# Performance work log

Hardware: AMD Instinct MI355X
Metric: run time of the kernel (lower is better)

## Reference

```python
import jax, jax.numpy as jnp
import numpy as np

N, L, M, NNZ, P, G, H = 4096, 64, 256, 100000, 3, 1, 8
D = M // H  # head_dim = 32


def setup_inputs() -> dict:
    key = jax.random.key(0)
    ks = jax.random.split(key, 8)
    return {
        "sparse_values": jax.random.normal(ks[0], (NNZ, M), jnp.float32),
        "linear_index": jax.random.randint(ks[1], (N, L), 0, NNZ, jnp.int32),
        "is_specified": jax.random.randint(ks[2], (N, L), 0, 2, jnp.int32).astype(bool),
        "query": jax.random.normal(ks[3], (N, M), jnp.float32),
        "key_weight": jax.random.normal(ks[4], (M, M), jnp.float32) * 0.05,
        "value_weight": jax.random.normal(ks[5], (M, M), jnp.float32) * 0.05,
        "key_positions": jax.random.uniform(ks[6], (N, L, P), jnp.float32),
        "rope_freqs": jax.random.normal(ks[7], (P, G, H, D // 2), jnp.float32),
        "n_heads": H,
    }


def reference(sparse_values, linear_index, is_specified, query, key_weight,
              value_weight, key_positions, rope_freqs, n_heads):
    n, l = linear_index.shape
    m = query.shape[-1]
    h = n_heads
    d = m // h
    scale = 1.0 / np.sqrt(m)  # docstring: default scale_factor = 1/sqrt(M)

    # Gather each query's key subset; unspecified keys -> 0 (will be masked)
    safe_idx = jnp.where(is_specified, linear_index, 0)
    gathered = jnp.where(is_specified[..., None], sparse_values[safe_idx], 0.0)  # [N,L,M]

    # Key / value projections (nn.Linear convention: x @ W.T)
    k = (gathered @ key_weight.T).reshape(n, l, h, d)
    v = (gathered @ value_weight.T).reshape(n, l, h, d)

    # RoPE on keys: angles [N,L,H,D/2], summed over position dims P and freq groups G
    angles = jnp.einsum('nlp,pghd->nlhd', key_positions, rope_freqs)
    cos, sin = jnp.cos(angles), jnp.sin(angles)
    k_even, k_odd = k[..., 0::2], k[..., 1::2]
    k = jnp.stack([k_even * cos - k_odd * sin,
                   k_even * sin + k_odd * cos], axis=-1).reshape(n, l, h, d)

    # Per-query subset attention (query is pre-rotated per docstring)
    q = query.reshape(n, h, d)
    scores = jnp.einsum('nhd,nlhd->nhl', q, k) * scale
    scores = jnp.where(is_specified[:, None, :], scores, -jnp.inf)

    # Queries with all keys unspecified -> zero output (avoid NaN from all -inf)
    any_spec = is_specified.any(axis=-1)  # [N]
    attn = jax.nn.softmax(jnp.where(any_spec[:, None, None], scores, 0.0), axis=-1)
    out = jnp.einsum('nhl,nlhd->nhd', attn, v).reshape(n, m)
    out = jnp.where(any_spec[:, None], out, 0.0)
    return out, is_specified
```

## Files before the change

kernel.cpp:

```cpp
#include <hip/hip_runtime.h>
#include <math.h>

#define N_Q 4096
#define L_K 64
#define M_D 256

typedef float f32x16 __attribute__((ext_vector_type(16)));
typedef __bf16 b16x8 __attribute__((ext_vector_type(8)));
union F8 { uint4 u; unsigned short s[8]; b16x8 v; };

__device__ __forceinline__ unsigned short f2bf(float x) {
  unsigned u = __float_as_uint(x);
  return (unsigned short)((u + 0x7fffu + ((u >> 16) & 1u)) >> 16);
}

__global__ __launch_bounds__(256) void k_prep(const unsigned char* __restrict__ raw,
                                              float* __restrict__ out2,
                                              const float* __restrict__ wv,
                                              float* __restrict__ wvt,
                                              const float* __restrict__ wk,
                                              unsigned short* __restrict__ wkf,
                                              const int* __restrict__ lin,
                                              int* __restrict__ pcnt,
                                              int* __restrict__ plin,
                                              unsigned char* __restrict__ pl) {
  __shared__ int pll_s[256];
  __shared__ unsigned char pls_s[256];
  __shared__ int pc_s[4];
  const int tid = threadIdx.x, lane = tid & 63;
  pll_s[tid] = 0;
  pls_s[tid] = 0;
  int v = 0;
  for (int i = tid; i < 4096; i += 256)
    if (i & 3) v |= raw[i];
  int f = __syncthreads_or(v);
  const int gi = blockIdx.x * 256 + tid;
  bool b = f ? (raw[gi] != 0) : (((const int*)raw)[gi] != 0);
  out2[gi] = b ? 1.0f : 0.0f;
  int li = lin[gi];
  unsigned long long mask = __ballot(b);
  if (b) {
    int rank = __popcll(mask & ((1ull << lane) - 1));
    pll_s[(tid & 192) + rank] = li;
    pls_s[(tid & 192) + rank] = (unsigned char)lane;
  }
  if (lane == 0) pc_s[tid >> 6] = __popcll(mask);
  __syncthreads();
  plin[gi] = pll_s[tid];
  pl[gi] = pls_s[tid];
  if (tid < 4) pcnt[blockIdx.x * 4 + tid] = pc_s[tid];

  if (gi < 65536) {
    wvt[(gi & 255) * 256 + (gi >> 8)] = wv[gi];
    int oc = gi >> 8, k = gi & 255;
    int tt = oc >> 5, c32o = oc & 31;
    int ks = k >> 4, kg2 = (k >> 3) & 1, j = k & 7;
    wkf[(((tt * 16 + ks) << 6) + kg2 * 32 + c32o) * 8 + j] = f2bf(wk[gi]);
  }
}

#define SC_OFF  65536
#define AT_OFF  (SC_OFF + 4096)
#define LDS_SZ  (AT_OFF + 4096)

__global__ __launch_bounds__(512, 4) void k_fused2(
    const float* __restrict__ sv, const float* __restrict__ q,
    const unsigned short* __restrict__ wkf, const float* __restrict__ pos,
    const float* __restrict__ freqs, const int* __restrict__ pcnt,
    const int* __restrict__ plin, const unsigned char* __restrict__ pl,
    unsigned short* __restrict__ agg) {
  __shared__ __align__(16) char smem[LDS_SZ];
  float* sc_s   = (float*)(smem + SC_OFF);
  float* attn_s = (float*)(smem + AT_OFF);
  const int tid = threadIdx.x, lane = tid & 63, w = tid >> 6;
  const int c32 = lane & 31, kg = lane >> 5;
  const int rt = w >> 1, ch = w & 1;
  const int n0g = blockIdx.x * 2;
  const int cnt0 = pcnt[n0g], cnt1 = pcnt[n0g + 1];
  const int cpair = cnt0 + cnt1;

  if (cpair == 0) {
    #pragma unroll
    for (int i = tid; i < 1024; i += 512)
      *(ushort4*)(agg + (size_t)n0g * 2048 + i * 4) = ushort4{0, 0, 0, 0};
    return;
  }
  const int ct32 = (cpair + 31) & ~31;
  const int ntiles = ct32 >> 5;

  {
    const int r0 = tid >> 5, ii = tid & 31;
    #pragma unroll
    for (int pp = 0; pp < 8; ++pp) {
      const int rloc = pp * 16 + r0;
      if (rloc < ct32) {
        const int pe = (rloc < cpair) ? rloc : (cpair - 1);
        const int src = (pe < cnt0) ? plin[n0g * 64 + pe]
                                    : plin[(n0g + 1) * 64 + (pe - cnt0)];
        const float* rp = sv + (size_t)src * 256 + ii * 8;
        float4 f0 = *(const float4*)rp;
        float4 f1 = *(const float4*)(rp + 4);
        F8 pk;
        pk.s[0] = f2bf(f0.x); pk.s[1] = f2bf(f0.y); pk.s[2] = f2bf(f0.z); pk.s[3] = f2bf(f0.w);
        pk.s[4] = f2bf(f1.x); pk.s[5] = f2bf(f1.y); pk.s[6] = f2bf(f1.z); pk.s[7] = f2bf(f1.w);
        *(uint4*)(smem + rloc * 512 + ((ii ^ (rloc & 31)) << 4)) = pk.u;
      }
    }
  }
  __syncthreads();

  if (rt < ntiles) {
    f32x16 acc[4];
    #pragma unroll
    for (int t = 0; t < 4; ++t)
      #pragma unroll
      for (int r = 0; r < 16; ++r) acc[t][r] = 0.0f;

    const char* fbase = (const char*)wkf + ch * 65536 + lane * 16;
    F8 afc[4], afn[4];
    #pragma unroll
    for (int t = 0; t < 4; ++t) afc[t].u = *(const uint4*)(fbase + (t * 16) * 1024);

    #pragma unroll
    for (int ks = 0; ks < 16; ++ks) {
      if (ks < 15) {
        #pragma unroll
        for (int t = 0; t < 4; ++t)
          afn[t].u = *(const uint4*)(fbase + (t * 16 + ks + 1) * 1024);
      }
      F8 bf;
      bf.u = *(const uint4*)(smem + (rt * 32 + c32) * 512 + ((((ks << 1) + kg) ^ c32) << 4));
      #pragma unroll
      for (int t = 0; t < 4; ++t)
        acc[t] = __builtin_amdgcn_mfma_f32_32x32x16_bf16(afc[t].v, bf.v, acc[t], 0, 0, 0);
      #pragma unroll
      for (int t = 0; t < 4; ++t) afc[t] = afn[t];
    }

    const int p = rt * 32 + c32;
    const bool pv = p < cpair;
    const int pe = pv ? p : (cpair - 1);
    const int nl = (pe >= cnt0) ? 1 : 0;
    const int n_g = n0g + nl;
    const int l = pl[n_g * 64 + (pe - (nl ? cnt0 : 0))];
    const float* lp = pos + ((size_t)n_g * 64 + l) * 3;
    const float pp0 = lp[0], pp1 = lp[1], pp2 = lp[2];
    #pragma unroll
    for (int t = 0; t < 4; ++t) {
      const int h = ch * 4 + t;
      const float* qh = q + (size_t)n_g * 256 + h * 32;
      const float* F = freqs + h * 16;
      float s = 0.f;
      #pragma unroll
      for (int g = 0; g < 4; ++g) {
        #pragma unroll
        for (int pr = 0; pr < 2; ++pr) {
          const int d0 = g * 8 + kg * 4 + pr * 2;
          const int jj = d0 >> 1;
          const int r = g * 4 + pr * 2;
          float ke = acc[t][r], ko = acc[t][r + 1];
          float ang = pp0 * F[jj] + pp1 * F[128 + jj] + pp2 * F[256 + jj];
          float sn, cs;
          __sincosf(ang, &sn, &cs);
          float2 qq = *(const float2*)(qh + d0);
          s += ke * (cs * qq.x + sn * qq.y) + ko * (cs * qq.y - sn * qq.x);
        }
      }
      s += __shfl_xor(s, 32);
      if (kg == 0 && pv) sc_s[p * 8 + h] = s * 0.0625f;
    }
  }
  __syncthreads();

  #pragma unroll
  for (int uu = 0; uu < 2; ++uu) {
    const int unit = w * 2 + uu;
    const int nl = unit >> 3, h = unit & 7;
    const int start = nl ? cnt0 : 0;
    const int cn = nl ? cnt1 : cnt0;
    const bool vl = lane < cn;
    float v = vl ? sc_s[(start + lane) * 8 + h] : -__builtin_inff();
    float mx = v;
    #pragma unroll
    for (int o = 32; o; o >>= 1) mx = fmaxf(mx, __shfl_xor(mx, o));
    float e = vl ? __expf(v - mx) : 0.f;
    float sm = e;
    #pragma unroll
    for (int o = 32; o; o >>= 1) sm += __shfl_xor(sm, o);
    if (vl) attn_s[(start + lane) * 8 + h] = e / sm;
  }
  __syncthreads();

  const int m = tid & 255, hh = tid >> 8;
  const int start = hh ? cnt0 : 0;
  const int cn = hh ? cnt1 : cnt0;
  const int n_g = n0g + hh;
  float ga[8];
  #pragma unroll
  for (int h = 0; h < 8; ++h) ga[h] = 0.f;
  for (int p2 = 0; p2 < cn; ++p2) {
    const int prow = start + p2;
    unsigned short us = *(const unsigned short*)(smem + prow * 512 +
                        ((((m >> 3) ^ (prow & 31)) << 4) | ((m & 7) << 1)));
    float gv = __uint_as_float((unsigned)us << 16);
    const float4* ap = (const float4*)(attn_s + prow * 8);
    float4 aA = ap[0], aB = ap[1];
    ga[0] += aA.x * gv; ga[1] += aA.y * gv; ga[2] += aA.z * gv; ga[3] += aA.w * gv;
    ga[4] += aB.x * gv; ga[5] += aB.y * gv; ga[6] += aB.z * gv; ga[7] += aB.w * gv;
  }
  #pragma unroll
  for (int h = 0; h < 8; ++h)
    agg[(size_t)n_g * 2048 + h * 256 + m] = f2bf(ga[h]);
}

__global__ __launch_bounds__(256) void k_out(const unsigned short* __restrict__ agg,
                                             const float* __restrict__ wvt,
                                             float* __restrict__ out) {
  __shared__ float a_s[4][8][260];
  const int tid = threadIdx.x;
  const int n0 = blockIdx.x * 4;
  #pragma unroll
  for (int it = 0; it < 4; ++it) {
    uint4 v = *(const uint4*)(agg + (size_t)(n0 + it) * 2048 + tid * 8);
    const unsigned short* sp = (const unsigned short*)&v;
    const int hh = tid >> 5, m0 = (tid & 31) * 8;
    #pragma unroll
    for (int k2 = 0; k2 < 8; ++k2)
      a_s[it][hh][m0 + k2] = __uint_as_float((unsigned)sp[k2] << 16);
  }
  __syncthreads();
  const int m = tid, h = m >> 5;
  float o0 = 0.f, o1 = 0.f, o2 = 0.f, o3 = 0.f;
  #pragma unroll 8
  for (int j = 0; j < 256; ++j) {
    float wvv = wvt[j * 256 + m];
    o0 += a_s[0][h][j] * wvv;
    o1 += a_s[1][h][j] * wvv;
    o2 += a_s[2][h][j] * wvv;
    o3 += a_s[3][h][j] * wvv;
  }
  out[(n0 + 0) * 256 + m] = o0;
  out[(n0 + 1) * 256 + m] = o1;
  out[(n0 + 2) * 256 + m] = o2;
  out[(n0 + 3) * 256 + m] = o3;
}

extern "C" void kernel_launch(void* const* d_in, const int* in_sizes, int n_in,
                              void* d_out, int out_size, void* d_ws, size_t ws_size,
                              hipStream_t stream) {
  const float* sv  = (const float*)d_in[0];
  const int* lin   = (const int*)d_in[1];
  const unsigned char* raw = (const unsigned char*)d_in[2];
  const float* q   = (const float*)d_in[3];
  const float* wk  = (const float*)d_in[4];
  const float* wv  = (const float*)d_in[5];
  const float* pos = (const float*)d_in[6];
  const float* fq  = (const float*)d_in[7];
  float* out = (float*)d_out;
  char* ws = (char*)d_ws;

  float* wvt          = (float*)ws;
  unsigned short* wkf = (unsigned short*)(ws + 262144);
  int* pcnt           = (int*)(ws + 393216);
  int* plin           = (int*)(ws + 409600);
  unsigned char* pl   = (unsigned char*)(ws + 1458176);
  unsigned short* agg = (unsigned short*)(ws + 1720320);

  k_prep  <<<1024, 256, 0, stream>>>(raw, out + N_Q * M_D, wv, wvt, wk, wkf,
                                     lin, pcnt, plin, pl);
  k_fused2<<<2048, 512, 0, stream>>>(sv, q, wkf, pos, fq, pcnt, plin, pl, agg);
  k_out   <<<1024, 256, 0, stream>>>(agg, wvt, out);
}
```

Measured before the change: 108.8 us.

## Process one query per 256-thread block instead of query pairs

Restructures the fused attention kernel so each block handles a single query with 256 threads and half the LDS, instead of packing two queries' keys into one 512-thread block. This removes the pair-indexing logic and allows more resident blocks per CU. The cost is wasted MFMA tile padding when a query's key count is not a multiple of 32, since pairs can no longer share tiles. It also hoists the position loads ahead of the barrier, splits sincos into separate sin/cos calls, and unrolls the aggregation loop.

New measurement: 107.8 us. About the same (-0.9%).

```diff
diff --git a/kernel.cpp b/kernel.cpp
--- a/kernel.cpp
+++ b/kernel.cpp
@@ -59,11 +59,11 @@
   }
 }
 
-#define SC_OFF  65536
-#define AT_OFF  (SC_OFF + 4096)
-#define LDS_SZ  (AT_OFF + 4096)
-
-__global__ __launch_bounds__(512, 4) void k_fused2(
+#define SC_OFF  32768
+#define AT_OFF  (SC_OFF + 2048)
+#define LDS_SZ  (AT_OFF + 2048)
+
+__global__ __launch_bounds__(256, 4) void k_fused3(
     const float* __restrict__ sv, const float* __restrict__ q,
     const unsigned short* __restrict__ wkf, const float* __restrict__ pos,
     const float* __restrict__ freqs, const int* __restrict__ pcnt,
@@ -75,29 +75,24 @@
   const int tid = threadIdx.x, lane = tid & 63, w = tid >> 6;
   const int c32 = lane & 31, kg = lane >> 5;
   const int rt = w >> 1, ch = w & 1;
-  const int n0g = blockIdx.x * 2;
-  const int cnt0 = pcnt[n0g], cnt1 = pcnt[n0g + 1];
-  const int cpair = cnt0 + cnt1;
-
-  if (cpair == 0) {
-    #pragma unroll
-    for (int i = tid; i < 1024; i += 512)
-      *(ushort4*)(agg + (size_t)n0g * 2048 + i * 4) = ushort4{0, 0, 0, 0};
+  const int n = blockIdx.x;
+  const int cnt = pcnt[n];
+
+  if (cnt == 0) {
+    *(uint4*)((char*)agg + (size_t)n * 4096 + tid * 16) = uint4{0, 0, 0, 0};
     return;
   }
-  const int ct32 = (cpair + 31) & ~31;
+  const int ct32 = (cnt + 31) & ~31;
   const int ntiles = ct32 >> 5;
 
   {
     const int r0 = tid >> 5, ii = tid & 31;
     #pragma unroll
     for (int pp = 0; pp < 8; ++pp) {
-      const int rloc = pp * 16 + r0;
+      const int rloc = pp * 8 + r0;
       if (rloc < ct32) {
-        const int pe = (rloc < cpair) ? rloc : (cpair - 1);
-        const int src = (pe < cnt0) ? plin[n0g * 64 + pe]
-                                    : plin[(n0g + 1) * 64 + (pe - cnt0)];
-        const float* rp = sv + (size_t)src * 256 + ii * 8;
+        const int pe = (rloc < cnt) ? rloc : (cnt - 1);
+        const float* rp = sv + (size_t)plin[n * 64 + pe] * 256 + ii * 8;
         float4 f0 = *(const float4*)rp;
         float4 f1 = *(const float4*)(rp + 4);
         F8 pk;
@@ -107,6 +102,14 @@
       }
     }
   }
+
+  const int p = rt * 32 + c32;
+  const bool pv = p < cnt;
+  const int pe2 = pv ? p : (cnt - 1);
+  const int l = pl[n * 64 + pe2];
+  const float* lp = pos + ((size_t)n * 64 + l) * 3;
+  const float pp0 = lp[0], pp1 = lp[1], pp2 = lp[2];
+
   __syncthreads();
 
   if (rt < ntiles) {
@@ -137,18 +140,10 @@
       for (int t = 0; t < 4; ++t) afc[t] = afn[t];
     }
 
-    const int p = rt * 32 + c32;
-    const bool pv = p < cpair;
-    const int pe = pv ? p : (cpair - 1);
-    const int nl = (pe >= cnt0) ? 1 : 0;
-    const int n_g = n0g + nl;
-    const int l = pl[n_g * 64 + (pe - (nl ? cnt0 : 0))];
-    const float* lp = pos + ((size_t)n_g * 64 + l) * 3;
-    const float pp0 = lp[0], pp1 = lp[1], pp2 = lp[2];
     #pragma unroll
     for (int t = 0; t < 4; ++t) {
       const int h = ch * 4 + t;
-      const float* qh = q + (size_t)n_g * 256 + h * 32;
+      const float* qh = q + (size_t)n * 256 + h * 32;
       const float* F = freqs + h * 16;
       float s = 0.f;
       #pragma unroll
@@ -160,8 +155,7 @@
           const int r = g * 4 + pr * 2;
           float ke = acc[t][r], ko = acc[t][r + 1];
           float ang = pp0 * F[jj] + pp1 * F[128 + jj] + pp2 * F[256 + jj];
-          float sn, cs;
-          __sincosf(ang, &sn, &cs);
+          float sn = __sinf(ang), cs = __cosf(ang);
           float2 qq = *(const float2*)(qh + d0);
           s += ke * (cs * qq.x + sn * qq.y) + ko * (cs * qq.y - sn * qq.x);
         }
@@ -174,12 +168,9 @@
 
   #pragma unroll
   for (int uu = 0; uu < 2; ++uu) {
-    const int unit = w * 2 + uu;
-    const int nl = unit >> 3, h = unit & 7;
-    const int start = nl ? cnt0 : 0;
-    const int cn = nl ? cnt1 : cnt0;
-    const bool vl = lane < cn;
-    float v = vl ? sc_s[(start + lane) * 8 + h] : -__builtin_inff();
+    const int h = w * 2 + uu;
+    const bool vl = lane < cnt;
+    float v = vl ? sc_s[lane * 8 + h] : -__builtin_inff();
     float mx = v;
     #pragma unroll
     for (int o = 32; o; o >>= 1) mx = fmaxf(mx, __shfl_xor(mx, o));
@@ -187,30 +178,27 @@
     float sm = e;
     #pragma unroll
     for (int o = 32; o; o >>= 1) sm += __shfl_xor(sm, o);
-    if (vl) attn_s[(start + lane) * 8 + h] = e / sm;
-  }
-  __syncthreads();
-
-  const int m = tid & 255, hh = tid >> 8;
-  const int start = hh ? cnt0 : 0;
-  const int cn = hh ? cnt1 : cnt0;
-  const int n_g = n0g + hh;
+    if (vl) attn_s[lane * 8 + h] = e / sm;
+  }
+  __syncthreads();
+
+  const int m = tid;
   float ga[8];
   #pragma unroll
   for (int h = 0; h < 8; ++h) ga[h] = 0.f;
-  for (int p2 = 0; p2 < cn; ++p2) {
-    const int prow = start + p2;
-    unsigned short us = *(const unsigned short*)(smem + prow * 512 +
-                        ((((m >> 3) ^ (prow & 31)) << 4) | ((m & 7) << 1)));
+  #pragma unroll 4
+  for (int p2 = 0; p2 < cnt; ++p2) {
+    unsigned short us = *(const unsigned short*)(smem + p2 * 512 +
+                        ((((m >> 3) ^ (p2 & 31)) << 4) | ((m & 7) << 1)));
     float gv = __uint_as_float((unsigned)us << 16);
-    const float4* ap = (const float4*)(attn_s + prow * 8);
+    const float4* ap = (const float4*)(attn_s + p2 * 8);
     float4 aA = ap[0], aB = ap[1];
     ga[0] += aA.x * gv; ga[1] += aA.y * gv; ga[2] += aA.z * gv; ga[3] += aA.w * gv;
     ga[4] += aB.x * gv; ga[5] += aB.y * gv; ga[6] += aB.z * gv; ga[7] += aB.w * gv;
   }
   #pragma unroll
   for (int h = 0; h < 8; ++h)
-    agg[(size_t)n_g * 2048 + h * 256 + m] = f2bf(ga[h]);
+    agg[(size_t)n * 2048 + h * 256 + m] = f2bf(ga[h]);
 }
 
 __global__ __launch_bounds__(256) void k_out(const unsigned short* __restrict__ agg,
@@ -268,6 +256,6 @@
 
   k_prep  <<<1024, 256, 0, stream>>>(raw, out + N_Q * M_D, wv, wvt, wk, wkf,
                                      lin, pcnt, plin, pl);
-  k_fused2<<<2048, 512, 0, stream>>>(sv, q, wkf, pos, fq, pcnt, plin, pl, agg);
+  k_fused3<<<4096, 256, 0, stream>>>(sv, q, wkf, pos, fq, pcnt, plin, pl, agg);
   k_out   <<<1024, 256, 0, stream>>>(agg, wvt, out);
 }
```

## Remap fused attention warps to one head each over all row tiles

Applied to the files above, without the earlier changes.

The fused key-projection/score kernel used to assign each warp one 32-row tile and four heads, holding four weight fragments. Now each warp owns a single head and loops over up to four row tiles, reusing one weight fragment across tiles. Each query's rows are padded to a 32-row tile boundary so tiles never mix queries, and positions are loaded before the barrier. This reduces weight-fragment loads and idle warps when there are few tiles, but can need more tiles for odd counts and drops the early exit for empty pairs. sincos is split into separate sin and cos calls, and the aggregation loop is unrolled.

New measurement: 112.8 us. 3.7% more time.

```diff
diff --git a/kernel.cpp b/kernel.cpp
--- a/kernel.cpp
+++ b/kernel.cpp
@@ -63,7 +63,7 @@
 #define AT_OFF  (SC_OFF + 4096)
 #define LDS_SZ  (AT_OFF + 4096)
 
-__global__ __launch_bounds__(512, 4) void k_fused2(
+__global__ __launch_bounds__(512, 4) void k_fused4(
     const float* __restrict__ sv, const float* __restrict__ q,
     const unsigned short* __restrict__ wkf, const float* __restrict__ pos,
     const float* __restrict__ freqs, const int* __restrict__ pcnt,
@@ -74,30 +74,22 @@
   float* attn_s = (float*)(smem + AT_OFF);
   const int tid = threadIdx.x, lane = tid & 63, w = tid >> 6;
   const int c32 = lane & 31, kg = lane >> 5;
-  const int rt = w >> 1, ch = w & 1;
   const int n0g = blockIdx.x * 2;
   const int cnt0 = pcnt[n0g], cnt1 = pcnt[n0g + 1];
-  const int cpair = cnt0 + cnt1;
-
-  if (cpair == 0) {
-    #pragma unroll
-    for (int i = tid; i < 1024; i += 512)
-      *(ushort4*)(agg + (size_t)n0g * 2048 + i * 4) = ushort4{0, 0, 0, 0};
-    return;
-  }
-  const int ct32 = (cpair + 31) & ~31;
-  const int ntiles = ct32 >> 5;
+  const int nt0 = (cnt0 + 31) >> 5, nt1 = (cnt1 + 31) >> 5;
+  const int ttot = nt0 + nt1;
+  const int nrows = ttot << 5;
 
   {
     const int r0 = tid >> 5, ii = tid & 31;
     #pragma unroll
     for (int pp = 0; pp < 8; ++pp) {
       const int rloc = pp * 16 + r0;
-      if (rloc < ct32) {
-        const int pe = (rloc < cpair) ? rloc : (cpair - 1);
-        const int src = (pe < cnt0) ? plin[n0g * 64 + pe]
-                                    : plin[(n0g + 1) * 64 + (pe - cnt0)];
-        const float* rp = sv + (size_t)src * 256 + ii * 8;
+      if (rloc < nrows) {
+        int pe, nsel;
+        if (rloc < (nt0 << 5)) { nsel = n0g;     pe = min(rloc, cnt0 - 1); }
+        else                   { nsel = n0g + 1; pe = min(rloc - (nt0 << 5), cnt1 - 1); }
+        const float* rp = sv + (size_t)plin[nsel * 64 + pe] * 256 + ii * 8;
         float4 f0 = *(const float4*)rp;
         float4 f1 = *(const float4*)(rp + 4);
         F8 pk;
@@ -107,49 +99,56 @@
       }
     }
   }
-  __syncthreads();
-
-  if (rt < ntiles) {
-    f32x16 acc[4];
-    #pragma unroll
-    for (int t = 0; t < 4; ++t)
-      #pragma unroll
-      for (int r = 0; r < 16; ++r) acc[t][r] = 0.0f;
-
-    const char* fbase = (const char*)wkf + ch * 65536 + lane * 16;
-    F8 afc[4], afn[4];
-    #pragma unroll
-    for (int t = 0; t < 4; ++t) afc[t].u = *(const uint4*)(fbase + (t * 16) * 1024);
-
-    #pragma unroll
-    for (int ks = 0; ks < 16; ++ks) {
-      if (ks < 15) {
-        #pragma unroll
-        for (int t = 0; t < 4; ++t)
-          afn[t].u = *(const uint4*)(fbase + (t * 16 + ks + 1) * 1024);
+
+  int   ng_r[4]; bool pv_r[4];
+  float p0_r[4], p1_r[4], p2_r[4];
+  #pragma unroll
+  for (int rt = 0; rt < 4; ++rt) {
+    const int slot = (rt << 5) + c32;
+    const bool in0 = rt < nt0;
+    const int n_g = in0 ? n0g : n0g + 1;
+    const int cn = in0 ? cnt0 : cnt1;
+    const int p = in0 ? slot : slot - (nt0 << 5);
+    const bool pv = (rt < ttot) && (p < cn);
+    const int pe2 = pv ? p : 0;
+    const int l = pl[n_g * 64 + pe2];
+    const float* lp = pos + ((size_t)n_g * 64 + l) * 3;
+    ng_r[rt] = n_g; pv_r[rt] = pv;
+    p0_r[rt] = lp[0]; p1_r[rt] = lp[1]; p2_r[rt] = lp[2];
+  }
+
+  __syncthreads();
+
+  f32x16 acc[4];
+  #pragma unroll
+  for (int rt = 0; rt < 4; ++rt)
+    #pragma unroll
+    for (int r = 0; r < 16; ++r) acc[rt][r] = 0.0f;
+
+  const char* fb = (const char*)wkf + (w << 14) + lane * 16;
+  F8 afc, afn;
+  afc.u = *(const uint4*)fb;
+  #pragma unroll
+  for (int ks = 0; ks < 16; ++ks) {
+    if (ks < 15) afn.u = *(const uint4*)(fb + (ks + 1) * 1024);
+    const int sl = (((ks << 1) + kg) ^ c32) << 4;
+    #pragma unroll
+    for (int rt = 0; rt < 4; ++rt) {
+      if (rt < ttot) {
+        F8 bf;
+        bf.u = *(const uint4*)(smem + ((rt << 5) + c32) * 512 + sl);
+        acc[rt] = __builtin_amdgcn_mfma_f32_32x32x16_bf16(afc.v, bf.v, acc[rt], 0, 0, 0);
       }
-      F8 bf;
-      bf.u = *(const uint4*)(smem + (rt * 32 + c32) * 512 + ((((ks << 1) + kg) ^ c32) << 4));
-      #pragma unroll
-      for (int t = 0; t < 4; ++t)
-        acc[t] = __builtin_amdgcn_mfma_f32_32x32x16_bf16(afc[t].v, bf.v, acc[t], 0, 0, 0);
-      #pragma unroll
-      for (int t = 0; t < 4; ++t) afc[t] = afn[t];
     }
-
-    const int p = rt * 32 + c32;
-    const bool pv = p < cpair;
-    const int pe = pv ? p : (cpair - 1);
-    const int nl = (pe >= cnt0) ? 1 : 0;
-    const int n_g = n0g + nl;
-    const int l = pl[n_g * 64 + (pe - (nl ? cnt0 : 0))];
-    const float* lp = pos + ((size_t)n_g * 64 + l) * 3;
-    const float pp0 = lp[0], pp1 = lp[1], pp2 = lp[2];
-    #pragma unroll
-    for (int t = 0; t < 4; ++t) {
-      const int h = ch * 4 + t;
-      const float* qh = q + (size_t)n_g * 256 + h * 32;
-      const float* F = freqs + h * 16;
+    afc = afn;
+  }
+
+  const float* F = freqs + w * 16;
+  #pragma unroll
+  for (int rt = 0; rt < 4; ++rt) {
+    if (rt < ttot) {
+      const float* qh = q + (size_t)ng_r[rt] * 256 + w * 32;
+      const float pp0 = p0_r[rt], pp1 = p1_r[rt], pp2 = p2_r[rt];
       float s = 0.f;
       #pragma unroll
       for (int g = 0; g < 4; ++g) {
@@ -158,16 +157,15 @@
           const int d0 = g * 8 + kg * 4 + pr * 2;
           const int jj = d0 >> 1;
           const int r = g * 4 + pr * 2;
-          float ke = acc[t][r], ko = acc[t][r + 1];
+          float ke = acc[rt][r], ko = acc[rt][r + 1];
           float ang = pp0 * F[jj] + pp1 * F[128 + jj] + pp2 * F[256 + jj];
-          float sn, cs;
-          __sincosf(ang, &sn, &cs);
+          float sn = __sinf(ang), cs = __cosf(ang);
           float2 qq = *(const float2*)(qh + d0);
           s += ke * (cs * qq.x + sn * qq.y) + ko * (cs * qq.y - sn * qq.x);
         }
       }
       s += __shfl_xor(s, 32);
-      if (kg == 0 && pv) sc_s[p * 8 + h] = s * 0.0625f;
+      if (kg == 0 && pv_r[rt]) sc_s[((rt << 5) + c32) * 8 + w] = s * 0.0625f;
     }
   }
   __syncthreads();
@@ -176,7 +174,7 @@
   for (int uu = 0; uu < 2; ++uu) {
     const int unit = w * 2 + uu;
     const int nl = unit >> 3, h = unit & 7;
-    const int start = nl ? cnt0 : 0;
+    const int start = nl ? (nt0 << 5) : 0;
     const int cn = nl ? cnt1 : cnt0;
     const bool vl = lane < cn;
     float v = vl ? sc_s[(start + lane) * 8 + h] : -__builtin_inff();
@@ -192,18 +190,19 @@
   __syncthreads();
 
   const int m = tid & 255, hh = tid >> 8;
-  const int start = hh ? cnt0 : 0;
+  const int start = hh ? (nt0 << 5) : 0;
   const int cn = hh ? cnt1 : cnt0;
   const int n_g = n0g + hh;
   float ga[8];
   #pragma unroll
   for (int h = 0; h < 8; ++h) ga[h] = 0.f;
+  #pragma unroll 4
   for (int p2 = 0; p2 < cn; ++p2) {
-    const int prow = start + p2;
-    unsigned short us = *(const unsigned short*)(smem + prow * 512 +
-                        ((((m >> 3) ^ (prow & 31)) << 4) | ((m & 7) << 1)));
+    const int row = start + p2;
+    unsigned short us = *(const unsigned short*)(smem + row * 512 +
+                        ((((m >> 3) ^ (row & 31)) << 4) | ((m & 7) << 1)));
     float gv = __uint_as_float((unsigned)us << 16);
-    const float4* ap = (const float4*)(attn_s + prow * 8);
+    const float4* ap = (const float4*)(attn_s + row * 8);
     float4 aA = ap[0], aB = ap[1];
     ga[0] += aA.x * gv; ga[1] += aA.y * gv; ga[2] += aA.z * gv; ga[3] += aA.w * gv;
     ga[4] += aB.x * gv; ga[5] += aB.y * gv; ga[6] += aB.z * gv; ga[7] += aB.w * gv;
@@ -268,6 +267,6 @@
 
   k_prep  <<<1024, 256, 0, stream>>>(raw, out + N_Q * M_D, wv, wvt, wk, wkf,
                                      lin, pcnt, plin, pl);
-  k_fused2<<<2048, 512, 0, stream>>>(sv, q, wkf, pos, fq, pcnt, plin, pl, agg);
+  k_fused4<<<2048, 512, 0, stream>>>(sv, q, wkf, pos, fq, pcnt, plin, pl, agg);
   k_out   <<<1024, 256, 0, stream>>>(agg, wvt, out);
 }
```
